# Optimization experiments

Measured on AMD Instinct MI355X. Metric: run time of the kernel, lower is better.

Reference implementation:

```python
import jax, jax.numpy as jnp
import numpy as np

N, E, DIM = 50000, 1600000, 64
EPS = 1e-5


def setup_inputs() -> dict:
    key = jax.random.key(0)
    ks = jax.random.split(key, 12)
    s = 1.0 / np.sqrt(3 * DIM)
    s1 = 1.0 / np.sqrt(DIM)
    return {
        "x": jax.random.normal(ks[0], (N, DIM), dtype=jnp.float32),
        "edge_index": jax.random.randint(ks[1], (2, E), 0, N, dtype=jnp.int64),
        "edge_attr": jax.random.normal(ks[2], (E, DIM), dtype=jnp.float32),
        # gate_linear: Linear(3*dim, dim)
        "Wg": jax.random.uniform(ks[3], (3 * DIM, DIM), jnp.float32, -s, s),
        "bg": jax.random.uniform(ks[4], (DIM,), jnp.float32, -s, s),
        # src_linear / dst_linear: Linear(dim, dim)
        "Ws": jax.random.uniform(ks[5], (DIM, DIM), jnp.float32, -s1, s1),
        "bs": jax.random.uniform(ks[6], (DIM,), jnp.float32, -s1, s1),
        "Wd": jax.random.uniform(ks[7], (DIM, DIM), jnp.float32, -s1, s1),
        "bd": jax.random.uniform(ks[8], (DIM,), jnp.float32, -s1, s1),
        # BatchNorm affine params (track_running_stats=False -> batch stats)
        "gamma_n": 1.0 + 0.1 * jax.random.normal(ks[9], (DIM,), dtype=jnp.float32),
        "beta_n": 0.1 * jax.random.normal(ks[10], (DIM,), dtype=jnp.float32),
        "gamma_e": 1.0 + 0.1 * jax.random.normal(ks[11], (DIM,), dtype=jnp.float32),
        "beta_e": 0.1 * jax.random.normal(jax.random.fold_in(key, 99), (DIM,), dtype=jnp.float32),
    }


def batch_norm(h, gamma, beta):
    # BatchNorm1d with track_running_stats=False: batch mean, biased variance
    mu = jnp.mean(h, axis=0)
    var = jnp.mean((h - mu) ** 2, axis=0)
    return (h - mu) * jax.lax.rsqrt(var + EPS) * gamma + beta


def reference(x, edge_index, edge_attr, Wg, bg, Ws, bs, Wd, bd,
              gamma_n, beta_n, gamma_e, beta_e):
    src_idx, dst_idx = edge_index[0], edge_index[1]
    # gate: Linear(cat([x[src], x[dst], edge_attr])) -- split matmul == concat matmul
    d = x.shape[1]
    m = (x[src_idx] @ Wg[:d] + x[dst_idx] @ Wg[d:2 * d] + edge_attr @ Wg[2 * d:] + bg)  # [E, d]
    sigma = jax.nn.sigmoid(m / jnp.sqrt(jnp.float32(d)))
    src = x @ Ws + bs                              # [N, d]
    dst = (x @ Wd + bd)[dst_idx]                   # linear-then-gather == gather-then-linear
    agg = jax.ops.segment_sum(sigma * dst, src_idx, num_segments=x.shape[0])  # [N, d]
    h = src + agg
    node_out = jax.nn.relu(batch_norm(h, gamma_n, beta_n))
    edge_out = jax.nn.relu(batch_norm(m, gamma_e, beta_e))
    return (node_out, edge_out)
```

## Files before the change

### kernel.cpp

```cpp
#include <hip/hip_runtime.h>



__global__ __launch_bounds__(256, 2) void node_kernel(
    const float* __restrict__ x,
    const float* __restrict__ Wg,
    const float* __restrict__ Ws, const float* __restrict__ bs,
    const float* __restrict__ Wd, const float* __restrict__ bd,
    float* __restrict__ g0, float* __restrict__ g1,
    float* __restrict__ srcL, float* __restrict__ dstL,
    int N, int ntiles)
{
    __shared__ float ldsA[4][4096];
    const int lane = threadIdx.x & 63;
    const int wid  = threadIdx.x >> 6;
    float* lds = ldsA[wid];
    const int nw = gridDim.x * 4;
    const float bsv = bs[lane], bdv = bd[lane];

    for (int tile = blockIdx.x * 4 + wid; tile < ntiles; tile += nw) {
        const int r0 = tile * 64;
        {
            const int rb = lane >> 5, c2 = lane & 31;
            #pragma unroll
            for (int i = 0; i < 32; ++i) {
                int r = 2 * i + rb;
                int row = r0 + r; if (row >= N) row = N - 1;
                float2 v = *reinterpret_cast<const float2*>(x + (size_t)row * 64 + 2 * c2);
                int p = ((c2 + r) & 31) << 1;
                *reinterpret_cast<float2*>(&lds[r * 64 + p]) = v;
            }
        }
        float xr[64];
        #pragma unroll
        for (int kk = 0; kk < 32; ++kk) {
            int p = ((kk + lane) & 31) << 1;
            float2 v = *reinterpret_cast<const float2*>(&lds[lane * 64 + p]);
            xr[2 * kk] = v.x; xr[2 * kk + 1] = v.y;
        }
        #pragma unroll 1
        for (int mt = 0; mt < 4; ++mt) {
            const float* __restrict__ Wm = (mt == 0) ? Wg : (mt == 1) ? (Wg + 4096)
                                         : (mt == 2) ? Ws : Wd;
            #pragma unroll 1
            for (int ct = 0; ct < 2; ++ct) {
                float acc[32];
                #pragma unroll
                for (int c = 0; c < 32; ++c) acc[c] = 0.f;
                const float* __restrict__ Wp = Wm + ct * 32;
                #pragma unroll
                for (int k = 0; k < 64; ++k) {
                    float a = xr[k];
                    #pragma unroll
                    for (int c = 0; c < 32; ++c)
                        acc[c] = fmaf(a, Wp[k * 64 + c], acc[c]);
                }
                #pragma unroll
                for (int cc = 0; cc < 16; ++cc) {
                    int q = ct * 16 + cc;
                    int p = ((q + lane) & 31) << 1;
                    *reinterpret_cast<float2*>(&lds[lane * 64 + p]) =
                        make_float2(acc[2 * cc], acc[2 * cc + 1]);
                }
            }
            float bv = (mt == 2) ? bsv : (mt == 3) ? bdv : 0.f;
            float* __restrict__ op = (mt == 0) ? g0 : (mt == 1) ? g1 : (mt == 2) ? srcL : dstL;
            for (int j = 0; j < 64; ++j) {
                int row = r0 + j;
                if (row >= N) break;
                int p = ((((lane >> 1) + j) & 31) << 1) | (lane & 1);
                op[(size_t)row * 64 + lane] = lds[j * 64 + p] + bv;
            }
        }
    }
}

__global__ __launch_bounds__(256, 2) void edge_kernel(
    const float* __restrict__ ea, const int* __restrict__ eidx,
    const float* __restrict__ W2, const float* __restrict__ bg,
    const float* __restrict__ g0, const float* __restrict__ g1,
    const float* __restrict__ dstL, float* __restrict__ m_out,
    float* __restrict__ agg, float* __restrict__ stats,
    int E, int ntiles)
{
    __shared__ float ldsA[4][4096];
    const int lane = threadIdx.x & 63;
    const int wid  = threadIdx.x >> 6;
    float* lds = ldsA[wid];
    const int nw = gridDim.x * 4;
    const float bgv = bg[lane];
    float ssum = 0.f, ssq = 0.f;

    for (int tile = blockIdx.x * 4 + wid; tile < ntiles; tile += nw) {
        const long e0 = (long)tile * 64;
        long el = e0 + lane; if (el >= E) el = E - 1;
        const int sv = eidx[el];
        const int dv = eidx[(long)E + el];

        {
            const int rb = lane >> 5, c2 = lane & 31;
            #pragma unroll
            for (int i = 0; i < 32; ++i) {
                int r = 2 * i + rb;
                long erow = e0 + r; if (erow >= E) erow = E - 1;
                float2 v = *reinterpret_cast<const float2*>(ea + erow * 64 + 2 * c2);
                int p = ((c2 + r) & 31) << 1;
                *reinterpret_cast<float2*>(&lds[r * 64 + p]) = v;
            }
        }
        float ear[64];
        #pragma unroll
        for (int kk = 0; kk < 32; ++kk) {
            int p = ((kk + lane) & 31) << 1;
            float2 v = *reinterpret_cast<const float2*>(&lds[lane * 64 + p]);
            ear[2 * kk] = v.x; ear[2 * kk + 1] = v.y;
        }
        #pragma unroll 1
        for (int ct = 0; ct < 2; ++ct) {
            float acc[32];
            #pragma unroll
            for (int c = 0; c < 32; ++c) acc[c] = 0.f;
            const float* __restrict__ Wp = W2 + ct * 32;
            #pragma unroll
            for (int k = 0; k < 64; ++k) {
                float a = ear[k];
                #pragma unroll
                for (int c = 0; c < 32; ++c)
                    acc[c] = fmaf(a, Wp[k * 64 + c], acc[c]);
            }
            #pragma unroll
            for (int cc = 0; cc < 16; ++cc) {
                int q = ct * 16 + cc;
                int p = ((q + lane) & 31) << 1;
                *reinterpret_cast<float2*>(&lds[lane * 64 + p]) =
                    make_float2(acc[2 * cc], acc[2 * cc + 1]);
            }
        }
        long rem = (long)E - e0;
        int jmax = rem < 64 ? (int)rem : 64;
        for (int j = 0; j < jmax; ++j) {
            int p = ((((lane >> 1) + j) & 31) << 1) | (lane & 1);
            float mv = lds[j * 64 + p];
            int s = __shfl(sv, j, 64);
            int d = __shfl(dv, j, 64);
            mv += bgv + g0[(size_t)s * 64 + lane] + g1[(size_t)d * 64 + lane];
            m_out[(e0 + j) * 64 + lane] = mv;
            ssum += mv;
            ssq = fmaf(mv, mv, ssq);
            float sg = __fdividef(1.f, 1.f + __expf(mv * -0.125f));
            float dl = dstL[(size_t)d * 64 + lane];
            atomicAdd(&agg[(size_t)s * 64 + lane], sg * dl);
        }
    }
    atomicAdd(&stats[lane], ssum);
    atomicAdd(&stats[64 + lane], ssq);
}

__global__ void node_stats_kernel(const float* __restrict__ srcL, const float* __restrict__ agg,
                                  float* __restrict__ stats, int N)
{
    const int lane = threadIdx.x & 63;
    const int wid  = threadIdx.x >> 6;
    const int w = blockIdx.x * 4 + wid, nw = gridDim.x * 4;
    float s = 0.f, q = 0.f;
    for (int row = w; row < N; row += nw) {
        float h = srcL[(size_t)row * 64 + lane] + agg[(size_t)row * 64 + lane];
        s += h; q = fmaf(h, h, q);
    }
    atomicAdd(&stats[128 + lane], s);
    atomicAdd(&stats[192 + lane], q);
}

__global__ void finalize_kernel(float* __restrict__ stats,
                                const float* __restrict__ gn, const float* __restrict__ bn,
                                const float* __restrict__ ge, const float* __restrict__ be,
                                float invE, float invN)
{
    int c = threadIdx.x;
    float mu = stats[c] * invE;
    float var = stats[64 + c] * invE - mu * mu;
    float rs = rsqrtf(var + 1e-5f);
    float sc = rs * ge[c];
    stats[256 + c] = sc;
    stats[320 + c] = be[c] - mu * sc;
    mu = stats[128 + c] * invN;
    var = stats[192 + c] * invN - mu * mu;
    rs = rsqrtf(var + 1e-5f);
    sc = rs * gn[c];
    stats[384 + c] = sc;
    stats[448 + c] = bn[c] - mu * sc;
}

__global__ void edge_norm_kernel(float* __restrict__ mbuf, const float* __restrict__ stats, long n4)
{
    long i = (long)blockIdx.x * blockDim.x + threadIdx.x;
    const long stride = (long)gridDim.x * blockDim.x;
    int c4 = (int)(i & 15) * 4;
    float4 sc = *reinterpret_cast<const float4*>(&stats[256 + c4]);
    float4 sh = *reinterpret_cast<const float4*>(&stats[320 + c4]);
    float4* p = reinterpret_cast<float4*>(mbuf);
    for (; i < n4; i += stride) {
        float4 v = p[i];
        v.x = fmaxf(fmaf(v.x, sc.x, sh.x), 0.f);
        v.y = fmaxf(fmaf(v.y, sc.y, sh.y), 0.f);
        v.z = fmaxf(fmaf(v.z, sc.z, sh.z), 0.f);
        v.w = fmaxf(fmaf(v.w, sc.w, sh.w), 0.f);
        p[i] = v;
    }
}

__global__ void node_norm_kernel(const float* __restrict__ srcL, const float* __restrict__ agg,
                                 const float* __restrict__ stats, float* __restrict__ out, long n4)
{
    long i = (long)blockIdx.x * blockDim.x + threadIdx.x;
    const long stride = (long)gridDim.x * blockDim.x;
    int c4 = (int)(i & 15) * 4;
    float4 sc = *reinterpret_cast<const float4*>(&stats[384 + c4]);
    float4 sh = *reinterpret_cast<const float4*>(&stats[448 + c4]);
    const float4* a = reinterpret_cast<const float4*>(srcL);
    const float4* b = reinterpret_cast<const float4*>(agg);
    float4* o = reinterpret_cast<float4*>(out);
    for (; i < n4; i += stride) {
        float4 va = a[i], vb = b[i];
        float4 v;
        v.x = fmaxf(fmaf(va.x + vb.x, sc.x, sh.x), 0.f);
        v.y = fmaxf(fmaf(va.y + vb.y, sc.y, sh.y), 0.f);
        v.z = fmaxf(fmaf(va.z + vb.z, sc.z, sh.z), 0.f);
        v.w = fmaxf(fmaf(va.w + vb.w, sc.w, sh.w), 0.f);
        o[i] = v;
    }
}

extern "C" void kernel_launch(void* const* d_in, const int* in_sizes, int n_in,
                              void* d_out, int out_size, void* d_ws, size_t ws_size,
                              hipStream_t stream)
{
    const float* x    = (const float*)d_in[0];
    const int*   eidx = (const int*)d_in[1];
    const float* ea   = (const float*)d_in[2];
    const float* Wg   = (const float*)d_in[3];
    const float* bg   = (const float*)d_in[4];
    const float* Ws   = (const float*)d_in[5];
    const float* bs   = (const float*)d_in[6];
    const float* Wd   = (const float*)d_in[7];
    const float* bd   = (const float*)d_in[8];
    const float* gn   = (const float*)d_in[9];
    const float* bn   = (const float*)d_in[10];
    const float* ge   = (const float*)d_in[11];
    const float* be   = (const float*)d_in[12];

    const int N = in_sizes[0] / 64;
    const int E = in_sizes[2] / 64;

    float* ws    = (float*)d_ws;
    size_t nb    = (size_t)N * 64;
    float* g0    = ws;
    float* g1    = ws + nb;
    float* srcL  = ws + 2 * nb;
    float* dstL  = ws + 3 * nb;
    float* agg   = ws + 4 * nb;
    float* stats = ws + 5 * nb;

    float* node_out = (float*)d_out;
    float* m_out    = node_out + nb;

    hipMemsetAsync(agg, 0, nb * sizeof(float), stream);
    hipMemsetAsync(stats, 0, 512 * sizeof(float), stream);

    const int ntilesN = (N + 63) / 64;
    node_kernel<<<196, 256, 0, stream>>>(x, Wg, Ws, bs, Wd, bd, g0, g1, srcL, dstL, N, ntilesN);

    const int ntilesE = (E + 63) / 64;
    edge_kernel<<<1568, 256, 0, stream>>>(ea, eidx, Wg + 128 * 64, bg, g0, g1, dstL,
                                          m_out, agg, stats, E, ntilesE);

    node_stats_kernel<<<256, 256, 0, stream>>>(srcL, agg, stats, N);
    finalize_kernel<<<1, 64, 0, stream>>>(stats, gn, bn, ge, be, 1.f / (float)E, 1.f / (float)N);

    edge_norm_kernel<<<4096, 256, 0, stream>>>(m_out, stats, (long)E * 16);
    node_norm_kernel<<<1024, 256, 0, stream>>>(srcL, agg, stats, node_out, (long)N * 16);
}
```

Measured before the change: 1.319 ms.

## Split edge tiles across a whole block with per-wave output column slices

```diff
diff --git a/kernel.cpp b/kernel.cpp
--- a/kernel.cpp
+++ b/kernel.cpp
@@ -75,7 +75,7 @@
     }
 }
 
-__global__ __launch_bounds__(256, 2) void edge_kernel(
+__global__ __launch_bounds__(256, 4) void edge_kernel(
     const float* __restrict__ ea, const int* __restrict__ eidx,
     const float* __restrict__ W2, const float* __restrict__ bg,
     const float* __restrict__ g0, const float* __restrict__ g1,
@@ -83,31 +83,25 @@
     float* __restrict__ agg, float* __restrict__ stats,
     int E, int ntiles)
 {
-    __shared__ float ldsA[4][4096];
-    const int lane = threadIdx.x & 63;
-    const int wid  = threadIdx.x >> 6;
-    float* lds = ldsA[wid];
-    const int nw = gridDim.x * 4;
+    __shared__ float lds[4096];
+    const int tid  = threadIdx.x;
+    const int lane = tid & 63;
+    const int wid  = __builtin_amdgcn_readfirstlane(tid >> 6);
     const float bgv = bg[lane];
     float ssum = 0.f, ssq = 0.f;
 
-    for (int tile = blockIdx.x * 4 + wid; tile < ntiles; tile += nw) {
+    for (int tile = blockIdx.x; tile < ntiles; tile += gridDim.x) {
         const long e0 = (long)tile * 64;
-        long el = e0 + lane; if (el >= E) el = E - 1;
-        const int sv = eidx[el];
-        const int dv = eidx[(long)E + el];
-
-        {
-            const int rb = lane >> 5, c2 = lane & 31;
-            #pragma unroll
-            for (int i = 0; i < 32; ++i) {
-                int r = 2 * i + rb;
-                long erow = e0 + r; if (erow >= E) erow = E - 1;
-                float2 v = *reinterpret_cast<const float2*>(ea + erow * 64 + 2 * c2);
-                int p = ((c2 + r) & 31) << 1;
-                *reinterpret_cast<float2*>(&lds[r * 64 + p]) = v;
-            }
-        }
+        #pragma unroll
+        for (int j = 0; j < 8; ++j) {
+            int fp = tid + j * 256;
+            int row = fp >> 5, c2 = fp & 31;
+            long erow = e0 + row; if (erow >= E) erow = E - 1;
+            float2 v = *reinterpret_cast<const float2*>(ea + erow * 64 + 2 * c2);
+            int p = ((c2 + row) & 31) << 1;
+            *reinterpret_cast<float2*>(&lds[row * 64 + p]) = v;
+        }
+        __syncthreads();
         float ear[64];
         #pragma unroll
         for (int kk = 0; kk < 32; ++kk) {
@@ -115,42 +109,45 @@
             float2 v = *reinterpret_cast<const float2*>(&lds[lane * 64 + p]);
             ear[2 * kk] = v.x; ear[2 * kk + 1] = v.y;
         }
-        #pragma unroll 1
-        for (int ct = 0; ct < 2; ++ct) {
-            float acc[32];
-            #pragma unroll
-            for (int c = 0; c < 32; ++c) acc[c] = 0.f;
-            const float* __restrict__ Wp = W2 + ct * 32;
+        __syncthreads();
+        {
+            float acc[16];
+            #pragma unroll
+            for (int c = 0; c < 16; ++c) acc[c] = 0.f;
+            const float* __restrict__ Wp = W2 + wid * 16;
             #pragma unroll
             for (int k = 0; k < 64; ++k) {
                 float a = ear[k];
                 #pragma unroll
-                for (int c = 0; c < 32; ++c)
+                for (int c = 0; c < 16; ++c)
                     acc[c] = fmaf(a, Wp[k * 64 + c], acc[c]);
             }
             #pragma unroll
-            for (int cc = 0; cc < 16; ++cc) {
-                int q = ct * 16 + cc;
+            for (int cc = 0; cc < 8; ++cc) {
+                int q = wid * 8 + cc;
                 int p = ((q + lane) & 31) << 1;
                 *reinterpret_cast<float2*>(&lds[lane * 64 + p]) =
                     make_float2(acc[2 * cc], acc[2 * cc + 1]);
             }
         }
-        long rem = (long)E - e0;
-        int jmax = rem < 64 ? (int)rem : 64;
-        for (int j = 0; j < jmax; ++j) {
+        __syncthreads();
+        #pragma unroll 4
+        for (int i = 0; i < 16; ++i) {
+            int j = wid * 16 + i;
+            long e = e0 + j;
+            if (e >= E) break;
+            int s = eidx[e];
+            int d = eidx[(long)E + e];
             int p = ((((lane >> 1) + j) & 31) << 1) | (lane & 1);
             float mv = lds[j * 64 + p];
-            int s = __shfl(sv, j, 64);
-            int d = __shfl(dv, j, 64);
             mv += bgv + g0[(size_t)s * 64 + lane] + g1[(size_t)d * 64 + lane];
-            m_out[(e0 + j) * 64 + lane] = mv;
+            m_out[e * 64 + lane] = mv;
             ssum += mv;
             ssq = fmaf(mv, mv, ssq);
             float sg = __fdividef(1.f, 1.f + __expf(mv * -0.125f));
-            float dl = dstL[(size_t)d * 64 + lane];
-            atomicAdd(&agg[(size_t)s * 64 + lane], sg * dl);
-        }
+            atomicAdd(&agg[(size_t)s * 64 + lane], sg * dstL[(size_t)d * 64 + lane]);
+        }
+        __syncthreads();
     }
     atomicAdd(&stats[lane], ssum);
     atomicAdd(&stats[64 + lane], ssq);
@@ -271,7 +268,7 @@
     node_kernel<<<196, 256, 0, stream>>>(x, Wg, Ws, bs, Wd, bd, g0, g1, srcL, dstL, N, ntilesN);
 
     const int ntilesE = (E + 63) / 64;
-    edge_kernel<<<1568, 256, 0, stream>>>(ea, eidx, Wg + 128 * 64, bg, g0, g1, dstL,
+    edge_kernel<<<2048, 256, 0, stream>>>(ea, eidx, Wg + 128 * 64, bg, g0, g1, dstL,
                                           m_out, agg, stats, E, ntilesE);
 
     node_stats_kernel<<<256, 256, 0, stream>>>(srcL, agg, stats, N);
```

Result: faster. 1.279 ms (-3.1%).
